# Kernel optimization log

Hardware: AMD Instinct MI355X
Metric: run time of the kernel (lower is better)

## Reference

```python
import jax, jax.numpy as jnp
import numpy as np

DIM = 1024
HEADS = 16
DIM_HEAD = 64
INNER = HEADS * DIM_HEAD
SEQ = 4096
BATCH = 1


def setup_inputs() -> dict:
    key = jax.random.key(0)
    ks = jax.random.split(key, 6)
    s = 0.02
    return {
        "x": jax.random.normal(ks[0], (BATCH, SEQ, DIM), dtype=jnp.float32),
        "Wq": jax.random.normal(ks[1], (DIM, INNER), dtype=jnp.float32) * s,
        "Wk": jax.random.normal(ks[2], (DIM, INNER), dtype=jnp.float32) * s,
        "Wv": jax.random.normal(ks[3], (DIM, INNER), dtype=jnp.float32) * s,
        "Wo": jax.random.normal(ks[4], (INNER, DIM), dtype=jnp.float32) * s,
        "bo": jax.random.normal(ks[5], (DIM,), dtype=jnp.float32) * s,
    }


def reference(x, Wq, Wk, Wv, Wo, bo):
    b, n, _ = x.shape
    beta = 1.0 / jnp.sqrt(jnp.float32(DIM_HEAD))
    # project and split heads: [b, n, inner] -> [b, h, n, d]
    def split_heads(t):
        return t.reshape(b, n, HEADS, DIM_HEAD).transpose(0, 2, 1, 3)
    q = split_heads(x @ Wq)
    k = split_heads(x @ Wk)
    v = split_heads(x @ Wv)
    # scaled scores [b, h, n, n]
    scores = jnp.einsum('bhid,bhjd->bhij', q * beta, k)
    mask_value = -jnp.finfo(scores.dtype).max
    causal = jnp.triu(jnp.ones((n, n), dtype=bool), k=1)
    scores = jnp.where(causal, mask_value, scores)
    attn = jax.nn.softmax(scores, axis=-1)
    out = jnp.einsum('bhij,bhjd->bhid', attn, v)
    out = out.transpose(0, 2, 1, 3).reshape(b, n, INNER)
    # output projection (dropout is identity in eval)
    return out @ Wo + bo
```

## Files before the change

kernel.cpp:

```cpp
#include <hip/hip_runtime.h>
#include <hip/hip_bf16.h>
#include <stdint.h>
#include <math.h>

#define SEQ 4096
#define DIM 1024
#define NHEADS 16
#define DHEAD 64
#define INNER 1024

typedef __hip_bfloat16 bf16;
typedef __attribute__((ext_vector_type(8))) short short8;
typedef __attribute__((ext_vector_type(4))) float floatx4;
typedef __attribute__((ext_vector_type(16))) float floatx16;

__device__ __forceinline__ void gll16(const bf16* g, bf16* l) {
    __builtin_amdgcn_global_load_lds(
        (const __attribute__((address_space(1))) unsigned int*)g,
        (__attribute__((address_space(3))) unsigned int*)l,
        16, 0, 0);
}

__device__ __forceinline__ unsigned short f2bf_bits(float f) {
    bf16 h = __float2bfloat16(f);
    return *reinterpret_cast<unsigned short*>(&h);
}

__device__ __forceinline__ uint2 pack4bf(float a, float b, float c, float d) {
    __hip_bfloat162 lo = __float22bfloat162_rn(float2{a, b});
    __hip_bfloat162 hi = __float22bfloat162_rn(float2{c, d});
    uint2 r;
    r.x = *reinterpret_cast<unsigned*>(&lo);
    r.y = *reinterpret_cast<unsigned*>(&hi);
    return r;
}

__device__ __forceinline__ unsigned pkbf(float lo, float hi) {
    __hip_bfloat162 h = __float22bfloat162_rn(float2{lo, hi});
    return *reinterpret_cast<unsigned*>(&h);
}

__global__ __launch_bounds__(256) void prep_kernel(
        const float* __restrict__ x, const float* __restrict__ W0,
        const float* __restrict__ W1, const float* __restrict__ W2,
        const float* __restrict__ W3, bf16* __restrict__ xb,
        bf16* __restrict__ T0, bf16* __restrict__ T1,
        bf16* __restrict__ T2, bf16* __restrict__ T3) {
    const int tid = threadIdx.x + threadIdx.y * blockDim.x;
    if (blockIdx.z == 4) {
        int chunk = blockIdx.y * 32 + blockIdx.x;
        int base = chunk * 4096 + tid * 4;
        #pragma unroll
        for (int r = 0; r < 4; r++) {
            int i = base + r * 1024;
            float4 f = *reinterpret_cast<const float4*>(x + i);
            unsigned long long p = (unsigned long long)f2bf_bits(f.x)
                                 | ((unsigned long long)f2bf_bits(f.y) << 16)
                                 | ((unsigned long long)f2bf_bits(f.z) << 32)
                                 | ((unsigned long long)f2bf_bits(f.w) << 48);
            *reinterpret_cast<unsigned long long*>(xb + i) = p;
        }
        return;
    }
    const float* W; bf16* T;
    switch (blockIdx.z) {
        case 0:  W = W0; T = T0; break;
        case 1:  W = W1; T = T1; break;
        case 2:  W = W2; T = T2; break;
        default: W = W3; T = T3; break;
    }
    __shared__ float tile[32][33];
    int k0 = blockIdx.x * 32, n0 = blockIdx.y * 32;
    int tx = threadIdx.x, ty = threadIdx.y;
    #pragma unroll
    for (int i = 0; i < 4; i++)
        tile[ty + 8 * i][tx] = W[(size_t)(k0 + ty + 8 * i) * 1024 + n0 + tx];
    __syncthreads();
    #pragma unroll
    for (int i = 0; i < 4; i++)
        T[(size_t)(n0 + ty + 8 * i) * 1024 + k0 + tx] = __float2bfloat16(tile[tx][ty + 8 * i]);
}

__device__ __forceinline__ void gemm128_body(const bf16* __restrict__ A,
                                             const bf16* __restrict__ Bt,
                                             int m0, int n0, floatx4 acc[4][4]) {
    __shared__ __align__(16) bf16 As[8192];
    __shared__ __align__(16) bf16 Bs[8192];
    const int tid = threadIdx.x;
    const int wave = tid >> 6;
    const int lane = tid & 63;
    const int l15 = lane & 15;
    const int quad = lane >> 4;

    #pragma unroll
    for (int i = 0; i < 4; i++)
        #pragma unroll
        for (int j = 0; j < 4; j++)
            acc[i][j] = (floatx4){0.f, 0.f, 0.f, 0.f};

    for (int k0 = 0; k0 < 1024; k0 += 64) {
        __syncthreads();
        #pragma unroll
        for (int j = 0; j < 4; j++) {
            int t = wave * 4 + j;
            int row = (t >> 1) * 16 + l15;
            int kb = (t & 1) * 32 + quad * 8;
            gll16(A + (size_t)(m0 + row) * 1024 + k0 + kb, &As[t * 512]);
            gll16(Bt + (size_t)(n0 + row) * 1024 + k0 + kb, &Bs[t * 512]);
        }
        __syncthreads();
        #pragma unroll
        for (int ks = 0; ks < 2; ks++) {
            short8 af[4], bfr[4];
            #pragma unroll
            for (int i = 0; i < 4; i++)
                af[i] = *reinterpret_cast<const short8*>(
                    &As[((((wave >> 1) * 4 + i) * 2 + ks) * 512) + lane * 8]);
            #pragma unroll
            for (int j = 0; j < 4; j++)
                bfr[j] = *reinterpret_cast<const short8*>(
                    &Bs[((((wave & 1) * 4 + j) * 2 + ks) * 512) + lane * 8]);
            #pragma unroll
            for (int i = 0; i < 4; i++)
                #pragma unroll
                for (int j = 0; j < 4; j++)
                    acc[i][j] = __builtin_amdgcn_mfma_f32_16x16x32_bf16(af[i], bfr[j], acc[i][j], 0, 0, 0);
        }
    }
}

__global__ __launch_bounds__(256) void qkv_gemm_kernel(
        const bf16* __restrict__ xb,
        const bf16* __restrict__ Wqt, const bf16* __restrict__ Wkt, const bf16* __restrict__ Wvt,
        bf16* __restrict__ Qh, bf16* __restrict__ Kh, bf16* __restrict__ Vt) {
    const bf16* Bt;
    if (blockIdx.z == 0)      Bt = Wqt;
    else if (blockIdx.z == 1) Bt = Wkt;
    else                      Bt = Wvt;
    int n0 = blockIdx.x * 128, m0 = blockIdx.y * 128;
    floatx4 acc[4][4];
    gemm128_body(xb, Bt, m0, n0, acc);

    const int tid = threadIdx.x, wave = tid >> 6, lane = tid & 63;
    const int l15 = lane & 15, quad = lane >> 4;
    const int wm = (wave >> 1) * 64, wn = (wave & 1) * 64;
    if (blockIdx.z == 2) {
        #pragma unroll
        for (int i = 0; i < 4; i++)
            #pragma unroll
            for (int j = 0; j < 4; j++) {
                int col = n0 + wn + j * 16 + l15;
                int h = col >> 6, d = col & 63;
                int row0 = m0 + wm + i * 16 + quad * 4;
                uint2 v = pack4bf(acc[i][j][0], acc[i][j][1], acc[i][j][2], acc[i][j][3]);
                *reinterpret_cast<uint2*>(Vt + ((size_t)h * DHEAD + d) * SEQ + row0) = v;
            }
    } else {
        bf16* O = (blockIdx.z == 0) ? Qh : Kh;
        float scale = (blockIdx.z == 0) ? 0.125f * 1.4426950408889634f : 1.0f;
        #pragma unroll
        for (int i = 0; i < 4; i++)
            #pragma unroll
            for (int j = 0; j < 4; j++) {
                int col = n0 + wn + j * 16 + l15;
                int h = col >> 6, d = col & 63;
                #pragma unroll
                for (int r = 0; r < 4; r++) {
                    int row = m0 + wm + i * 16 + quad * 4 + r;
                    O[((size_t)h * SEQ + row) * DHEAD + d] = __float2bfloat16(acc[i][j][r] * scale);
                }
            }
    }
}

__global__ __launch_bounds__(256) void out_gemm_kernel(
        const bf16* __restrict__ Oa, const bf16* __restrict__ Wot,
        const float* __restrict__ bo, float* __restrict__ out) {
    int n0 = blockIdx.x * 128, m0 = blockIdx.y * 128;
    floatx4 acc[4][4];
    gemm128_body(Oa, Wot, m0, n0, acc);

    const int tid = threadIdx.x, wave = tid >> 6, lane = tid & 63;
    const int l15 = lane & 15, quad = lane >> 4;
    const int wm = (wave >> 1) * 64, wn = (wave & 1) * 64;
    #pragma unroll
    for (int i = 0; i < 4; i++)
        #pragma unroll
        for (int j = 0; j < 4; j++) {
            int col = n0 + wn + j * 16 + l15;
            float b = bo[col];
            #pragma unroll
            for (int r = 0; r < 4; r++) {
                int row = m0 + wm + i * 16 + quad * 4 + r;
                out[(size_t)row * DIM + col] = acc[i][j][r] + b;
            }
        }
}

#define PV_STEP(P, KTG)                                                              \
    do {                                                                             \
        const int rb_ = ((KTG) & 1) * 8;                                             \
        unsigned A0_ = pkbf((P)[rb_ + 0], (P)[rb_ + 1]);                             \
        unsigned B0_ = pkbf((P)[rb_ + 4], (P)[rb_ + 5]);                             \
        unsigned A1_ = pkbf((P)[rb_ + 2], (P)[rb_ + 3]);                             \
        unsigned B1_ = pkbf((P)[rb_ + 6], (P)[rb_ + 7]);                             \
        asm("v_permlane32_swap_b32 %0, %1" : "+v"(A0_), "+v"(B0_));                  \
        asm("v_permlane32_swap_b32 %0, %1" : "+v"(A1_), "+v"(B1_));                  \
        uint4 w_; w_.x = A0_; w_.y = A1_; w_.z = B0_; w_.w = B1_;                    \
        short8 bp_ = *reinterpret_cast<short8*>(&w_);                                \
        short8 av0_ = *reinterpret_cast<const short8*>(                              \
            &Vsh[cur][(KTG) * 512 + lane * 8]);                                      \
        short8 av1_ = *reinterpret_cast<const short8*>(                              \
            &Vsh[cur][(4 + (KTG)) * 512 + lane * 8]);                                \
        acc0 = __builtin_amdgcn_mfma_f32_32x32x16_bf16(av0_, bp_, acc0, 0, 0, 0);    \
        acc1 = __builtin_amdgcn_mfma_f32_32x32x16_bf16(av1_, bp_, acc1, 0, 0, 0);    \
    } while (0)

__global__ __launch_bounds__(256, 4) void attention_kernel(
        const bf16* __restrict__ Qh, const bf16* __restrict__ Kh,
        const bf16* __restrict__ Vt, bf16* __restrict__ Oa,
        float* __restrict__ Op0, float* __restrict__ Op1,
        float* __restrict__ L0, float* __restrict__ L1) {
    __shared__ __align__(16) bf16 Ksh[2][4096];
    __shared__ __align__(16) bf16 Vsh[2][4096];
    const int tid = threadIdx.x, wave = tid >> 6, lane = tid & 63;
    const int ql = lane & 31, half = lane >> 5;
    const int h8 = half * 8;
    const int id = blockIdx.x;
    const int head = id & 15;
    const int rk = id >> 4;
    int t, ck;
    if (rk < 16)      { t = 16 + rk; ck = 0; }
    else if (rk < 32) { t = 47 - rk; ck = 1; }
    else              { t = rk - 32; ck = 0; }
    const bool split = (t >= 16);
    const int ktile0 = (split && ck == 1) ? 32 : 0;
    const int ktile1 = (split && ck == 0) ? 32 : (2 * t + 2);
    const int qw = t * 128 + wave * 32;
    const int q = qw + ql;
    const size_t hoff = (size_t)head * SEQ * DHEAD;
    const bf16* Qb = Qh + hoff;
    const bf16* Kb = Kh + hoff;
    const bf16* Vb = Vt + hoff;

    short8 bq[4];
    #pragma unroll
    for (int kc = 0; kc < 4; kc++)
        bq[kc] = *reinterpret_cast<const short8*>(
            Qb + (size_t)q * DHEAD + kc * 16 + h8);

    floatx16 acc0, acc1;
    #pragma unroll
    for (int r = 0; r < 16; r++) { acc0[r] = 0.f; acc1[r] = 0.f; }
    float l_part = 0.f;

    auto stage = [&](int buf, int kbase) {
        #pragma unroll
        for (int j = 0; j < 2; j++) {
            int tc = wave * 2 + j;
            gll16(Kb + (size_t)(kbase + (tc >> 2) * 32 + ql) * DHEAD + (tc & 3) * 16 + h8,
                  &Ksh[buf][tc * 512]);
            gll16(Vb + (size_t)((tc >> 2) * 32 + ql) * SEQ + kbase + (tc & 3) * 16 + h8,
                  &Vsh[buf][tc * 512]);
        }
    };

    stage(0, ktile0 * 64);
    __syncthreads();
    int cur = 0;
    for (int kt = ktile0; kt < ktile1; kt++) {
        const int kbase = kt * 64;
        if (kt + 1 < ktile1) stage(cur ^ 1, (kt + 1) * 64);

        floatx16 s0, s1;
        #pragma unroll
        for (int r = 0; r < 16; r++) { s0[r] = 0.f; s1[r] = 0.f; }
        __builtin_amdgcn_s_setprio(1);
        #pragma unroll
        for (int kc = 0; kc < 4; kc++) {
            short8 ak0 = *reinterpret_cast<const short8*>(&Ksh[cur][kc * 512 + lane * 8]);
            short8 ak1 = *reinterpret_cast<const short8*>(&Ksh[cur][(4 + kc) * 512 + lane * 8]);
            s0 = __builtin_amdgcn_mfma_f32_32x32x16_bf16(ak0, bq[kc], s0, 0, 0, 0);
            s1 = __builtin_amdgcn_mfma_f32_32x32x16_bf16(ak1, bq[kc], s1, 0, 0, 0);
        }
        __builtin_amdgcn_s_setprio(0);
        if (kbase + 63 > qw) {
            int base0 = kbase + half * 4 - q;
            #pragma unroll
            for (int r = 0; r < 16; r++) {
                int off = (r & 3) + 8 * (r >> 2);
                if (base0 + off > 0)      s0[r] = -1e30f;
                if (base0 + 32 + off > 0) s1[r] = -1e30f;
            }
        }
        #pragma unroll
        for (int r = 0; r < 16; r++) {
            s0[r] = __builtin_amdgcn_exp2f(s0[r]);
            s1[r] = __builtin_amdgcn_exp2f(s1[r]);
            l_part += s0[r] + s1[r];
        }
        __builtin_amdgcn_s_setprio(1);
        PV_STEP(s0, 0); PV_STEP(s0, 1); PV_STEP(s1, 2); PV_STEP(s1, 3);
        __builtin_amdgcn_s_setprio(0);

        __syncthreads();
        cur ^= 1;
    }
    float l = l_part + __shfl_xor(l_part, 32, 64);
    if (!split) {
        float rcp = 1.0f / l;
        #pragma unroll
        for (int a = 0; a < 4; a++) {
            int d0 = 8 * a + half * 4;
            uint2 v0 = pack4bf(acc0[4 * a + 0] * rcp, acc0[4 * a + 1] * rcp,
                               acc0[4 * a + 2] * rcp, acc0[4 * a + 3] * rcp);
            *reinterpret_cast<uint2*>(Oa + (size_t)q * INNER + head * DHEAD + d0) = v0;
            uint2 v1 = pack4bf(acc1[4 * a + 0] * rcp, acc1[4 * a + 1] * rcp,
                               acc1[4 * a + 2] * rcp, acc1[4 * a + 3] * rcp);
            *reinterpret_cast<uint2*>(Oa + (size_t)q * INNER + head * DHEAD + 32 + d0) = v1;
        }
    } else {
        float* Op = ck ? Op1 : Op0;
        float* Lp = ck ? L1 : L0;
        if (half == 0) Lp[head * 2048 + (q - 2048)] = l;
        #pragma unroll
        for (int a = 0; a < 4; a++) {
            int d0 = 8 * a + half * 4;
            floatx4 v0 = {acc0[4 * a + 0], acc0[4 * a + 1], acc0[4 * a + 2], acc0[4 * a + 3]};
            *reinterpret_cast<floatx4*>(
                Op + (size_t)(q - 2048) * INNER + head * DHEAD + d0) = v0;
            floatx4 v1 = {acc1[4 * a + 0], acc1[4 * a + 1], acc1[4 * a + 2], acc1[4 * a + 3]};
            *reinterpret_cast<floatx4*>(
                Op + (size_t)(q - 2048) * INNER + head * DHEAD + 32 + d0) = v1;
        }
    }
}

__global__ __launch_bounds__(256) void combine_kernel(
        const float* __restrict__ Op0, const float* __restrict__ Op1,
        const float* __restrict__ L0, const float* __restrict__ L1,
        bf16* __restrict__ Oa) {
    int idx = blockIdx.x * 256 + threadIdx.x;
    int row = idx >> 8;
    int c4 = (idx & 255) * 4;
    int head = c4 >> 6;
    float l = L0[head * 2048 + row] + L1[head * 2048 + row];
    float rcp = 1.0f / l;
    float4 a = *reinterpret_cast<const float4*>(Op0 + (size_t)row * INNER + c4);
    float4 b = *reinterpret_cast<const float4*>(Op1 + (size_t)row * INNER + c4);
    uint2 v = pack4bf((a.x + b.x) * rcp, (a.y + b.y) * rcp,
                      (a.z + b.z) * rcp, (a.w + b.w) * rcp);
    *reinterpret_cast<uint2*>(Oa + (size_t)(2048 + row) * INNER + c4) = v;
}

extern "C" void kernel_launch(void* const* d_in, const int* in_sizes, int n_in,
                              void* d_out, int out_size, void* d_ws, size_t ws_size,
                              hipStream_t stream) {
    const float* x  = (const float*)d_in[0];
    const float* Wq = (const float*)d_in[1];
    const float* Wk = (const float*)d_in[2];
    const float* Wv = (const float*)d_in[3];
    const float* Wo = (const float*)d_in[4];
    const float* bo = (const float*)d_in[5];
    float* out = (float*)d_out;

    char* ws = (char*)d_ws;
    size_t off = 0;
    bf16* xb  = (bf16*)(ws + off); off += (size_t)SEQ * DIM * 2;
    bf16* Wqt = (bf16*)(ws + off); off += (size_t)DIM * INNER * 2;
    bf16* Wkt = (bf16*)(ws + off); off += (size_t)DIM * INNER * 2;
    bf16* Wvt = (bf16*)(ws + off); off += (size_t)DIM * INNER * 2;
    bf16* Wot = (bf16*)(ws + off); off += (size_t)INNER * DIM * 2;
    bf16* Qh  = (bf16*)(ws + off); off += (size_t)NHEADS * SEQ * DHEAD * 2;
    bf16* Kh  = (bf16*)(ws + off); off += (size_t)NHEADS * SEQ * DHEAD * 2;
    bf16* Vtr = (bf16*)(ws + off); off += (size_t)NHEADS * DHEAD * SEQ * 2;
    bf16* Oa  = (bf16*)(ws + off); off += (size_t)SEQ * INNER * 2;
    float* Op0 = (float*)(ws + off); off += (size_t)(SEQ / 2) * INNER * 4;
    float* Op1 = (float*)(ws + off); off += (size_t)(SEQ / 2) * INNER * 4;
    float* L0  = (float*)(ws + off); off += (size_t)NHEADS * (SEQ / 2) * 4;
    float* L1  = (float*)(ws + off); off += (size_t)NHEADS * (SEQ / 2) * 4;

    prep_kernel<<<dim3(32, 32, 5), dim3(32, 8), 0, stream>>>(x, Wq, Wk, Wv, Wo,
                                                             xb, Wqt, Wkt, Wvt, Wot);
    qkv_gemm_kernel<<<dim3(8, 32, 3), 256, 0, stream>>>(xb, Wqt, Wkt, Wvt, Qh, Kh, Vtr);
    attention_kernel<<<768, 256, 0, stream>>>(Qh, Kh, Vtr, Oa, Op0, Op1, L0, L1);
    combine_kernel<<<2048, 256, 0, stream>>>(Op0, Op1, L0, L1, Oa);
    out_gemm_kernel<<<dim3(8, 32), 256, 0, stream>>>(Oa, Wot, bo, out);
}
```

Measured before the change: 237.4 us.

## Load GEMM fragments directly from global memory, dropping LDS staging

The QKV and output-projection GEMMs no longer stage A and B tiles through shared memory with global_load_lds and barriers. Each wave now loads its MFMA fragments straight from global memory into registers, and the launch bounds request 3 blocks per CU. The goal is to remove LDS traffic and __syncthreads stalls. In exchange, each wave loads its own fragments, so global and L2 traffic rises because the tile loads that the block shared before are repeated across waves, and register pressure goes up.

```diff
diff --git a/kernel.cpp b/kernel.cpp
--- a/kernel.cpp
+++ b/kernel.cpp
@@ -81,17 +81,18 @@
         T[(size_t)(n0 + ty + 8 * i) * 1024 + k0 + tx] = __float2bfloat16(tile[tx][ty + 8 * i]);
 }
 
-__device__ __forceinline__ void gemm128_body(const bf16* __restrict__ A,
-                                             const bf16* __restrict__ Bt,
-                                             int m0, int n0, floatx4 acc[4][4]) {
-    __shared__ __align__(16) bf16 As[8192];
-    __shared__ __align__(16) bf16 Bs[8192];
+__device__ __forceinline__ void gemm128_direct(const bf16* __restrict__ A,
+                                               const bf16* __restrict__ Bt,
+                                               int m0, int n0, floatx4 acc[4][4]) {
     const int tid = threadIdx.x;
     const int wave = tid >> 6;
     const int lane = tid & 63;
     const int l15 = lane & 15;
     const int quad = lane >> 4;
 
+    const bf16* Ab = A + (size_t)(m0 + (wave >> 1) * 64 + l15) * 1024 + quad * 8;
+    const bf16* Bb = Bt + (size_t)(n0 + (wave & 1) * 64 + l15) * 1024 + quad * 8;
+
     #pragma unroll
     for (int i = 0; i < 4; i++)
         #pragma unroll
@@ -99,37 +100,28 @@
             acc[i][j] = (floatx4){0.f, 0.f, 0.f, 0.f};
 
     for (int k0 = 0; k0 < 1024; k0 += 64) {
-        __syncthreads();
-        #pragma unroll
-        for (int j = 0; j < 4; j++) {
-            int t = wave * 4 + j;
-            int row = (t >> 1) * 16 + l15;
-            int kb = (t & 1) * 32 + quad * 8;
-            gll16(A + (size_t)(m0 + row) * 1024 + k0 + kb, &As[t * 512]);
-            gll16(Bt + (size_t)(n0 + row) * 1024 + k0 + kb, &Bs[t * 512]);
-        }
-        __syncthreads();
-        #pragma unroll
-        for (int ks = 0; ks < 2; ks++) {
-            short8 af[4], bfr[4];
-            #pragma unroll
-            for (int i = 0; i < 4; i++)
-                af[i] = *reinterpret_cast<const short8*>(
-                    &As[((((wave >> 1) * 4 + i) * 2 + ks) * 512) + lane * 8]);
-            #pragma unroll
-            for (int j = 0; j < 4; j++)
-                bfr[j] = *reinterpret_cast<const short8*>(
-                    &Bs[((((wave & 1) * 4 + j) * 2 + ks) * 512) + lane * 8]);
+        short8 af[2][4], bfr[2][4];
+        #pragma unroll
+        for (int ks = 0; ks < 2; ks++)
+            #pragma unroll
+            for (int i = 0; i < 4; i++) {
+                af[ks][i] = *reinterpret_cast<const short8*>(
+                    Ab + (size_t)i * 16 * 1024 + k0 + ks * 32);
+                bfr[ks][i] = *reinterpret_cast<const short8*>(
+                    Bb + (size_t)i * 16 * 1024 + k0 + ks * 32);
+            }
+        #pragma unroll
+        for (int ks = 0; ks < 2; ks++)
             #pragma unroll
             for (int i = 0; i < 4; i++)
                 #pragma unroll
                 for (int j = 0; j < 4; j++)
-                    acc[i][j] = __builtin_amdgcn_mfma_f32_16x16x32_bf16(af[i], bfr[j], acc[i][j], 0, 0, 0);
-        }
-    }
-}
-
-__global__ __launch_bounds__(256) void qkv_gemm_kernel(
+                    acc[i][j] = __builtin_amdgcn_mfma_f32_16x16x32_bf16(
+                        af[ks][i], bfr[ks][j], acc[i][j], 0, 0, 0);
+    }
+}
+
+__global__ __launch_bounds__(256, 3) void qkv_gemm_kernel(
         const bf16* __restrict__ xb,
         const bf16* __restrict__ Wqt, const bf16* __restrict__ Wkt, const bf16* __restrict__ Wvt,
         bf16* __restrict__ Qh, bf16* __restrict__ Kh, bf16* __restrict__ Vt) {
@@ -139,7 +131,7 @@
     else                      Bt = Wvt;
     int n0 = blockIdx.x * 128, m0 = blockIdx.y * 128;
     floatx4 acc[4][4];
-    gemm128_body(xb, Bt, m0, n0, acc);
+    gemm128_direct(xb, Bt, m0, n0, acc);
 
     const int tid = threadIdx.x, wave = tid >> 6, lane = tid & 63;
     const int l15 = lane & 15, quad = lane >> 4;
@@ -173,12 +165,12 @@
     }
 }
 
-__global__ __launch_bounds__(256) void out_gemm_kernel(
+__global__ __launch_bounds__(256, 3) void out_gemm_kernel(
         const bf16* __restrict__ Oa, const bf16* __restrict__ Wot,
         const float* __restrict__ bo, float* __restrict__ out) {
     int n0 = blockIdx.x * 128, m0 = blockIdx.y * 128;
     floatx4 acc[4][4];
-    gemm128_body(Oa, Wot, m0, n0, acc);
+    gemm128_direct(Oa, Wot, m0, n0, acc);
 
     const int tid = threadIdx.x, wave = tid >> 6, lane = tid & 63;
     const int l15 = lane & 15, quad = lane >> 4;
```

After: 277.1 us. 1.17x slower.
